# Kernel optimization log

Measured on AMD Instinct MI355X. Metric: run time of the kernel, lower is better.

## Reference

```python
import jax, jax.numpy as jnp
import numpy as np
from functools import partial

B, C, H, W = 32, 16, 256, 256
HIDDEN = 128
N_FILT = 3

SOBEL_X = jnp.array([[-1., 0., 1.], [-2., 0., 2.], [-1., 0., 1.]], dtype=jnp.float32)
SOBEL_Y = jnp.array([[-1., -2., -1.], [0., 0., 0.], [1., 2., 1.]], dtype=jnp.float32)
CELL_ID = jnp.array([[0., 0., 0.], [0., 1., 0.], [0., 0., 0.]], dtype=jnp.float32)
ALIVE_K = jnp.ones((1, 1, 3, 3), dtype=jnp.float32)


def _conv3x3_same(x, kernel):
    # x: [B, Cin, H, W], kernel: [Cout, Cin, 3, 3], padding=1
    return jax.lax.conv_general_dilated(
        x, kernel, window_strides=(1, 1), padding='SAME',
        dimension_numbers=('NCHW', 'OIHW', 'NCHW'))


def _perceive(x, k2d):
    # Original weight is k2d repeated to [16,16,3,3] (identical kernel for every
    # in/out channel pair), so conv2d(x, W) == conv2d(sum_c x_c, k2d) broadcast
    # to 16 identical output channels. Same math, far less work.
    xs = jnp.sum(x, axis=1, keepdims=True)            # [B,1,H,W]
    out = _conv3x3_same(xs, k2d[None, None, :, :])     # [B,1,H,W]
    return jnp.broadcast_to(out, (x.shape[0], C, x.shape[2], x.shape[3]))


def setup_inputs() -> dict:
    key = jax.random.key(0)
    k1, k2, k3 = jax.random.split(key, 3)
    x = jax.random.uniform(k1, (B, C, H, W), dtype=jnp.float32)
    random_mask = jax.random.randint(k2, (B, 1, H, W), 0, 2, dtype=jnp.int32)
    w1 = jax.random.normal(k3, (HIDDEN, N_FILT * C), dtype=jnp.float32) * 0.05
    b1 = jnp.zeros((HIDDEN,), dtype=jnp.float32)
    # NOTE: original inits fc2.weight to zeros; use small random so dx is nontrivial
    w2 = jax.random.normal(jax.random.fold_in(key, 7), (C, HIDDEN), dtype=jnp.float32) * 0.05
    b2 = jnp.zeros((C,), dtype=jnp.float32)
    return {'x': x, 'random_mask': random_mask, 'w1': w1, 'b1': b1, 'w2': w2, 'b2': b2}


def reference(x, random_mask, w1, b1, w2, b2):
    # perception: [sobelX, sobelY, cellId] blocks of 16 channels each -> [B,48,H,W]
    perception = jnp.concatenate(
        [_perceive(x, SOBEL_X), _perceive(x, SOBEL_Y), _perceive(x, CELL_ID)], axis=1)
    # 1x1 conv MLP
    h = jnp.einsum('oc,bchw->bohw', w1, perception) + b1[None, :, None, None]
    h = jax.nn.relu(h)
    dx = jnp.einsum('oc,bchw->bohw', w2, h) + b2[None, :, None, None]
    # stochastic update: mask broadcast over all 16 channels
    x_new = x + dx * random_mask.astype(x.dtype)
    # alive mask: 3x3 ones conv over (alpha > 0.1), then > 0, broadcast over channels
    alpha_alive = (x_new[:, 3:4, :, :] > 0.1).astype(x.dtype)  # [B,1,H,W]
    alive = _conv3x3_same(alpha_alive, ALIVE_K) > 0.0           # [B,1,H,W] bool
    return x_new * alive.astype(x.dtype)
```

## Files before the change

### kernel.cpp

```cpp
#include <hip/hip_runtime.h>
#include <hip/hip_fp16.h>

#define B_   32
#define C_   16
#define H_   256
#define W_   256
#define HW_  65536
#define HID_ 128
#define T_   8
#define NBLK_ (B_*H_/T_)

typedef __attribute__((ext_vector_type(8))) _Float16 f16x8;
typedef __attribute__((ext_vector_type(2))) _Float16 f16x2;
typedef __attribute__((ext_vector_type(4))) float    f32x4;

__device__ __forceinline__ int h2i(f16x2 h) { return __builtin_bit_cast(int, h); }
__device__ __forceinline__ f16x2 i2h(int i) { return __builtin_bit_cast(f16x2, i); }

__device__ __forceinline__ f16x2 pk(float a, float b) {
    f16x2 r; r.x = (_Float16)a; r.y = (_Float16)b; return r;
}

__global__ __launch_bounds__(128) void nca_prep(
    const float* __restrict__ w1, const float* __restrict__ b1,
    int4* __restrict__ coefH)
{
    __shared__ float4 tmp[128];
    int o = threadIdx.x;
    float A = 0.f, Bc = 0.f, Cc = 0.f;
    #pragma unroll
    for (int k = 0;  k < 16; ++k) A  += w1[o*48 + k];
    #pragma unroll
    for (int k = 16; k < 32; ++k) Bc += w1[o*48 + k];
    #pragma unroll
    for (int k = 32; k < 48; ++k) Cc += w1[o*48 + k];
    tmp[o] = make_float4(A, Bc, Cc, b1[o]);
    __syncthreads();
    if (o < 64) {
        float4 e = tmp[2*o], f = tmp[2*o+1];
        coefH[o] = make_int4(h2i(pk(e.x, f.x)), h2i(pk(e.y, f.y)),
                             h2i(pk(e.z, f.z)), h2i(pk(e.w, f.w)));
    }
}

__global__ __launch_bounds__(256, 3) void nca_fused(
    const float* __restrict__ x, const int* __restrict__ mask,
    const int4* __restrict__ coefH, const float* __restrict__ w2,
    const float* __restrict__ b2,
    float* __restrict__ out, unsigned char* __restrict__ alpha)
{
    __shared__ float srow[T_+2][W_];
    __shared__ short hlds[4*2048];

    const int tid  = threadIdx.x;
    const int lane = tid & 63;
    const int widx = tid >> 6;
    const int col  = tid;
    const int q = lane & 15;
    const int g = lane >> 4;

    const int blk = blockIdx.x;
    const int b   = blk >> 5;
    const int r0  = (blk & 31) * T_;

    const float* xb = x    + (size_t)b * C_ * HW_;
    const int*   mb = mask + (size_t)b * HW_;
    float*       ob = (float*)out + (size_t)b * C_ * HW_;
    unsigned char* ab = alpha + (size_t)b * HW_;

    f16x8 af2[4];
    #pragma unroll
    for (int kb = 0; kb < 4; ++kb) {
        const float* wp = w2 + q*HID_ + kb*32 + g*8;
        f16x8 a;
        #pragma unroll
        for (int j = 0; j < 8; ++j) a[j] = (_Float16)wp[j];
        af2[kb] = a;
    }
    f32x4 bias;
    #pragma unroll
    for (int r = 0; r < 4; ++r) bias[r] = b2[g*4 + r];

    float xnext[C_];
    {
        float s0 = 0.f;
        if (r0 > 0) {
            #pragma unroll
            for (int c = 0; c < C_; ++c) s0 += xb[c*HW_ + (r0-1)*W_ + col];
        }
        float s1 = 0.f;
        #pragma unroll
        for (int c = 0; c < C_; ++c) s1 += xb[c*HW_ + r0*W_ + col];
        #pragma unroll
        for (int c = 0; c < C_; ++c) xnext[c] = xb[c*HW_ + (r0+1)*W_ + col];
        srow[0][col] = s0;
        srow[1][col] = s1;
    }

    const int wswz = (lane ^ (lane >> 2)) & 3;
    const int rsw  = (q ^ (q >> 2)) & 3;
    short* hw = hlds + widx*2048;

    for (int r = 0; r < T_; ++r) {
        const int row = r0 + r;

        {
            float s = 0.f;
            #pragma unroll
            for (int c = 0; c < C_; ++c) s += xnext[c];
            srow[r+2][col] = s;
        }
        __syncthreads();

        if (r < T_-1) {
            const int nr = r0 + r + 2;
            if (nr < H_) {
                #pragma unroll
                for (int c = 0; c < C_; ++c) xnext[c] = xb[c*HW_ + nr*W_ + col];
            } else {
                #pragma unroll
                for (int c = 0; c < C_; ++c) xnext[c] = 0.f;
            }
        }

        const int pstrip = row*W_ + (widx << 6);
        float mv[4];
        #pragma unroll
        for (int t = 0; t < 4; ++t) mv[t] = (float)mb[pstrip + t*16 + q];

        const bool jm = col > 0, jp = col < W_-1;
        const float* sA = srow[r];
        const float* sB = srow[r+1];
        const float* sC = srow[r+2];
        float n00 = jm ? sA[col-1] : 0.f, n01 = sA[col], n02 = jp ? sA[col+1] : 0.f;
        float n10 = jm ? sB[col-1] : 0.f,                n12 = jp ? sB[col+1] : 0.f;
        float n20 = jm ? sC[col-1] : 0.f, n21 = sC[col], n22 = jp ? sC[col+1] : 0.f;
        float px = (n02 - n00) + 2.f*(n12 - n10) + (n22 - n20);
        float py = (n20 - n00) + 2.f*(n21 - n01) + (n22 - n02);
        float sc = sB[col];

        const f16x2 px2 = pk(px, px);
        const f16x2 py2 = pk(py, py);
        const f16x2 sc2 = pk(sc, sc);
        const f16x2 z2  = pk(0.f, 0.f);

        f32x4 acc[4];
        #pragma unroll
        for (int t = 0; t < 4; ++t) acc[t] = bias;

        #pragma unroll
        for (int kb = 0; kb < 4; ++kb) {
            #pragma unroll
            for (int c = 0; c < 4; ++c) {
                int hd[4];
                #pragma unroll
                for (int u = 0; u < 4; ++u) {
                    const int4 cw = coefH[kb*16 + c*4 + u];
                    f16x2 h2 = __builtin_elementwise_fma(i2h(cw.x), px2,
                               __builtin_elementwise_fma(i2h(cw.y), py2,
                               __builtin_elementwise_fma(i2h(cw.z), sc2,
                                                         i2h(cw.w))));
                    h2 = __builtin_elementwise_max(h2, z2);
                    hd[u] = h2i(h2);
                }
                *(int4*)(hw + lane*32 + ((c ^ wswz) << 3)) =
                    make_int4(hd[0], hd[1], hd[2], hd[3]);
            }
            __builtin_amdgcn_wave_barrier();
            #pragma unroll
            for (int t = 0; t < 4; ++t) {
                const int pp = t*16 + q;
                f16x8 hbf = *(const f16x8*)(hw + pp*32 + (((g ^ rsw) & 3) << 3));
                acc[t] = __builtin_amdgcn_mfma_f32_16x16x32_f16(
                             af2[kb], hbf, acc[t], 0, 0, 0);
            }
            __builtin_amdgcn_wave_barrier();
        }

        #pragma unroll
        for (int t = 0; t < 4; ++t) {
            const int pp = pstrip + t*16 + q;
            float xn3 = 0.f;
            #pragma unroll
            for (int e = 0; e < 4; ++e) {
                const int chn = g*4 + e;
                float xv = xb[chn*HW_ + pp];
                float xn = fmaf(acc[t][e], mv[t], xv);
                ob[chn*HW_ + pp] = xn;
                if (chn == 3) xn3 = xn;
            }
            if (g == 0) ab[pp] = (xn3 > 0.1f) ? (unsigned char)1
                                              : (unsigned char)0;
        }
    }
}

__global__ __launch_bounds__(256) void nca_alive(
    const unsigned char* __restrict__ alpha, float* __restrict__ out)
{
    int t = blockIdx.x * blockDim.x + threadIdx.x;
    if (t >= B_*HW_) return;
    int b = t >> 16;
    int p = t & (HW_-1);
    int i = p >> 8;
    int j = p & (W_-1);
    const unsigned char* ab = alpha + (size_t)b * HW_;

    bool im = i > 0, ip = i < H_-1, jm = j > 0, jp = j < W_-1;
    int acc = ab[p];
    acc += jm ? ab[p-1] : 0;
    acc += jp ? ab[p+1] : 0;
    if (im) {
        acc += ab[p-W_];
        acc += jm ? ab[p-W_-1] : 0;
        acc += jp ? ab[p-W_+1] : 0;
    }
    if (ip) {
        acc += ab[p+W_];
        acc += jm ? ab[p+W_-1] : 0;
        acc += jp ? ab[p+W_+1] : 0;
    }
    if (acc == 0) {
        size_t base = (size_t)b * C_ * HW_ + p;
        #pragma unroll
        for (int c = 0; c < C_; ++c) out[base + (size_t)c * HW_] = 0.f;
    }
}

extern "C" void kernel_launch(void* const* d_in, const int* in_sizes, int n_in,
                              void* d_out, int out_size, void* d_ws, size_t ws_size,
                              hipStream_t stream)
{
    const float* x    = (const float*)d_in[0];
    const int*   mask = (const int*)d_in[1];
    const float* w1   = (const float*)d_in[2];
    const float* b1   = (const float*)d_in[3];
    const float* w2   = (const float*)d_in[4];
    const float* b2   = (const float*)d_in[5];
    float* out = (float*)d_out;

    char* ws = (char*)d_ws;
    unsigned char* alpha = (unsigned char*)ws;
    int4*          coefH = (int4*)(ws + (size_t)B_*HW_);

    nca_prep<<<1, 128, 0, stream>>>(w1, b1, coefH);

    nca_fused<<<NBLK_, 256, 0, stream>>>(x, mask, coefH, w2, b2, out, alpha);

    int n = B_*HW_;
    nca_alive<<<(n + 255)/256, 256, 0, stream>>>(alpha, out);
}
```

Before: 101.3 us.

## Use per-wave row-sum rings with halo shuffles instead of block-wide shared rows

Each wave now keeps its own three-row ring of channel-summed values for its 64 columns, with the two halo columns produced by shuffle reductions. This removes the block-wide __syncthreads and the register prefetch of the next row. The fp16 conversion of w2 moves into the prep kernel and is read from global memory per k-block, which lowers register use. The row tile shrinks to 4 and occupancy is raised to 6 blocks. In exchange, each block reloads two more halo rows relative to the rows it computes, and the next row's loads are no longer overlapped with compute.

```diff
diff --git a/kernel.cpp b/kernel.cpp
--- a/kernel.cpp
+++ b/kernel.cpp
@@ -7,7 +7,7 @@
 #define W_   256
 #define HW_  65536
 #define HID_ 128
-#define T_   8
+#define T_   4
 #define NBLK_ (B_*H_/T_)
 
 typedef __attribute__((ext_vector_type(8))) _Float16 f16x8;
@@ -23,7 +23,8 @@
 
 __global__ __launch_bounds__(128) void nca_prep(
     const float* __restrict__ w1, const float* __restrict__ b1,
-    int4* __restrict__ coefH)
+    const float* __restrict__ w2,
+    int4* __restrict__ coefH, short* __restrict__ w2h)
 {
     __shared__ float4 tmp[128];
     int o = threadIdx.x;
@@ -41,108 +42,117 @@
         coefH[o] = make_int4(h2i(pk(e.x, f.x)), h2i(pk(e.y, f.y)),
                              h2i(pk(e.z, f.z)), h2i(pk(e.w, f.w)));
     }
-}
-
-__global__ __launch_bounds__(256, 3) void nca_fused(
+    for (int e = threadIdx.x; e < 256; e += 128) {
+        const int kb = e >> 6, l = e & 63;
+        const int qq = l & 15, gg = l >> 4;
+        const float* wp = w2 + qq*HID_ + kb*32 + gg*8;
+        f16x8 a;
+        #pragma unroll
+        for (int j = 0; j < 8; ++j) a[j] = (_Float16)wp[j];
+        *(f16x8*)(w2h + e*8) = a;
+    }
+}
+
+__global__ __launch_bounds__(256, 6) void nca_fused(
     const float* __restrict__ x, const int* __restrict__ mask,
-    const int4* __restrict__ coefH, const float* __restrict__ w2,
+    const int4* __restrict__ coefH, const short* __restrict__ w2h,
     const float* __restrict__ b2,
     float* __restrict__ out, unsigned char* __restrict__ alpha)
 {
-    __shared__ float srow[T_+2][W_];
     __shared__ short hlds[4*2048];
+    __shared__ float swave[4][3][66];
 
     const int tid  = threadIdx.x;
     const int lane = tid & 63;
     const int widx = tid >> 6;
     const int col  = tid;
+    const int c0   = widx << 6;
     const int q = lane & 15;
     const int g = lane >> 4;
 
     const int blk = blockIdx.x;
-    const int b   = blk >> 5;
-    const int r0  = (blk & 31) * T_;
+    const int b   = blk >> 6;
+    const int r0  = (blk & 63) * T_;
 
     const float* xb = x    + (size_t)b * C_ * HW_;
     const int*   mb = mask + (size_t)b * HW_;
     float*       ob = (float*)out + (size_t)b * C_ * HW_;
     unsigned char* ab = alpha + (size_t)b * HW_;
 
-    f16x8 af2[4];
-    #pragma unroll
-    for (int kb = 0; kb < 4; ++kb) {
-        const float* wp = w2 + q*HID_ + kb*32 + g*8;
-        f16x8 a;
-        #pragma unroll
-        for (int j = 0; j < 8; ++j) a[j] = (_Float16)wp[j];
-        af2[kb] = a;
-    }
+    float (*sw)[66] = swave[widx];
+
     f32x4 bias;
     #pragma unroll
     for (int r = 0; r < 4; ++r) bias[r] = b2[g*4 + r];
-
-    float xnext[C_];
-    {
-        float s0 = 0.f;
-        if (r0 > 0) {
-            #pragma unroll
-            for (int c = 0; c < C_; ++c) s0 += xb[c*HW_ + (r0-1)*W_ + col];
-        }
-        float s1 = 0.f;
-        #pragma unroll
-        for (int c = 0; c < C_; ++c) s1 += xb[c*HW_ + r0*W_ + col];
-        #pragma unroll
-        for (int c = 0; c < C_; ++c) xnext[c] = xb[c*HW_ + (r0+1)*W_ + col];
-        srow[0][col] = s0;
-        srow[1][col] = s1;
-    }
 
     const int wswz = (lane ^ (lane >> 2)) & 3;
     const int rsw  = (q ^ (q >> 2)) & 3;
     short* hw = hlds + widx*2048;
 
+    const int hc   = (lane < 16) ? (c0 - 1) : (c0 + 64);
+    const bool hok = (lane < 32) && (hc >= 0) && (hc < W_);
+
+    {
+        float s0 = 0.f, s1 = 0.f, h0 = 0.f, h1 = 0.f;
+        if (r0 > 0) {
+            #pragma unroll
+            for (int c = 0; c < C_; ++c) s0 += xb[c*HW_ + (r0-1)*W_ + col];
+            if (hok) h0 = xb[(lane & 15)*HW_ + (r0-1)*W_ + hc];
+        }
+        #pragma unroll
+        for (int c = 0; c < C_; ++c) s1 += xb[c*HW_ + r0*W_ + col];
+        if (hok) h1 = xb[(lane & 15)*HW_ + r0*W_ + hc];
+        #pragma unroll
+        for (int o = 1; o < 16; o <<= 1) {
+            h0 += __shfl_xor(h0, o);
+            h1 += __shfl_xor(h1, o);
+        }
+        sw[0][1+lane] = s0;
+        sw[1][1+lane] = s1;
+        if (lane == 0)  { sw[0][0]  = h0; sw[1][0]  = h1; }
+        if (lane == 16) { sw[0][65] = h0; sw[1][65] = h1; }
+    }
+    __builtin_amdgcn_wave_barrier();
+
     for (int r = 0; r < T_; ++r) {
-        const int row = r0 + r;
+        const int row  = r0 + r;
+        const int nr   = row + 1;
+        const int slot = (r + 2) % 3;
 
         {
-            float s = 0.f;
-            #pragma unroll
-            for (int c = 0; c < C_; ++c) s += xnext[c];
-            srow[r+2][col] = s;
-        }
-        __syncthreads();
-
-        if (r < T_-1) {
-            const int nr = r0 + r + 2;
+            float s = 0.f, hv = 0.f;
             if (nr < H_) {
                 #pragma unroll
-                for (int c = 0; c < C_; ++c) xnext[c] = xb[c*HW_ + nr*W_ + col];
-            } else {
-                #pragma unroll
-                for (int c = 0; c < C_; ++c) xnext[c] = 0.f;
-            }
-        }
-
-        const int pstrip = row*W_ + (widx << 6);
-        float mv[4];
-        #pragma unroll
-        for (int t = 0; t < 4; ++t) mv[t] = (float)mb[pstrip + t*16 + q];
-
-        const bool jm = col > 0, jp = col < W_-1;
-        const float* sA = srow[r];
-        const float* sB = srow[r+1];
-        const float* sC = srow[r+2];
-        float n00 = jm ? sA[col-1] : 0.f, n01 = sA[col], n02 = jp ? sA[col+1] : 0.f;
-        float n10 = jm ? sB[col-1] : 0.f,                n12 = jp ? sB[col+1] : 0.f;
-        float n20 = jm ? sC[col-1] : 0.f, n21 = sC[col], n22 = jp ? sC[col+1] : 0.f;
+                for (int c = 0; c < C_; ++c) s += xb[c*HW_ + nr*W_ + col];
+                if (hok) hv = xb[(lane & 15)*HW_ + nr*W_ + hc];
+            }
+            #pragma unroll
+            for (int o = 1; o < 16; o <<= 1) hv += __shfl_xor(hv, o);
+            sw[slot][1+lane] = s;
+            if (lane == 0)  sw[slot][0]  = hv;
+            if (lane == 16) sw[slot][65] = hv;
+        }
+        __builtin_amdgcn_wave_barrier();
+
+        const float* sAp = sw[(r    ) % 3];
+        const float* sBp = sw[(r + 1) % 3];
+        const float* sCp = sw[(r + 2) % 3];
+        float n00 = sAp[lane], n01 = sAp[lane+1], n02 = sAp[lane+2];
+        float n10 = sBp[lane],                    n12 = sBp[lane+2];
+        float n20 = sCp[lane], n21 = sCp[lane+1], n22 = sCp[lane+2];
         float px = (n02 - n00) + 2.f*(n12 - n10) + (n22 - n20);
         float py = (n20 - n00) + 2.f*(n21 - n01) + (n22 - n02);
-        float sc = sB[col];
+        float sc = sBp[lane+1];
 
         const f16x2 px2 = pk(px, px);
         const f16x2 py2 = pk(py, py);
         const f16x2 sc2 = pk(sc, sc);
         const f16x2 z2  = pk(0.f, 0.f);
+
+        const int pstrip = row*W_ + c0;
+        float mv[4];
+        #pragma unroll
+        for (int t = 0; t < 4; ++t) mv[t] = (float)mb[pstrip + t*16 + q];
 
         f32x4 acc[4];
         #pragma unroll
@@ -167,12 +177,13 @@
                     make_int4(hd[0], hd[1], hd[2], hd[3]);
             }
             __builtin_amdgcn_wave_barrier();
+            const f16x8 af = *(const f16x8*)(w2h + (kb*64 + lane)*8);
             #pragma unroll
             for (int t = 0; t < 4; ++t) {
                 const int pp = t*16 + q;
                 f16x8 hbf = *(const f16x8*)(hw + pp*32 + (((g ^ rsw) & 3) << 3));
                 acc[t] = __builtin_amdgcn_mfma_f32_16x16x32_f16(
-                             af2[kb], hbf, acc[t], 0, 0, 0);
+                             af, hbf, acc[t], 0, 0, 0);
             }
             __builtin_amdgcn_wave_barrier();
         }
@@ -192,6 +203,7 @@
             if (g == 0) ab[pp] = (xn3 > 0.1f) ? (unsigned char)1
                                               : (unsigned char)0;
         }
+        __builtin_amdgcn_wave_barrier();
     }
 }
 
@@ -242,10 +254,11 @@
     char* ws = (char*)d_ws;
     unsigned char* alpha = (unsigned char*)ws;
     int4*          coefH = (int4*)(ws + (size_t)B_*HW_);
-
-    nca_prep<<<1, 128, 0, stream>>>(w1, b1, coefH);
-
-    nca_fused<<<NBLK_, 256, 0, stream>>>(x, mask, coefH, w2, b2, out, alpha);
+    short*         w2h   = (short*)(ws + (size_t)B_*HW_ + 1024);
+
+    nca_prep<<<1, 128, 0, stream>>>(w1, b1, w2, coefH, w2h);
+
+    nca_fused<<<NBLK_, 256, 0, stream>>>(x, mask, coefH, w2h, b2, out, alpha);
 
     int n = B_*HW_;
     nca_alive<<<(n + 255)/256, 256, 0, stream>>>(alpha, out);
```

Measured after the change: 198.0 us. 95.5% more time.
